# Kernel tuning notes

Measured on AMD Instinct MI355X. Metric: run time of the kernel, lower is better.

Reference implementation:

```python
import jax, jax.numpy as jnp
import numpy as np

# Problem dims (see shape_source)
T, H, FFN, K, E = 2048, 1024, 2048, 4, 32
LOCAL_EXPERT_IDS = (0, 8, 16, 24)  # round_robin plan: E=32, ep_size=8, ep_rank=0
N_LOCAL = len(LOCAL_EXPERT_IDS)
W_INIT = 0.02


def setup_inputs() -> dict:
    key = jax.random.key(0)
    k1, k2, k3, k4, k5 = jax.random.split(key, 5)
    hidden_2d = jax.random.normal(k1, (T, H), jnp.float32)
    selected_experts = jax.random.randint(k2, (T, K), 0, E)          # int routing ids
    routing_weights = jax.random.uniform(k3, (T, K), jnp.float32)    # nonneg gate probs
    gate_up_stack = jax.random.normal(k4, (N_LOCAL, 2 * FFN, H), jnp.float32) * W_INIT
    down_stack = jax.random.normal(k5, (N_LOCAL, H, FFN), jnp.float32) * W_INIT
    return {
        "hidden_2d": hidden_2d,
        "selected_experts": selected_experts,
        "routing_weights": routing_weights,
        "gate_up_stack": gate_up_stack,
        "down_stack": down_stack,
    }


def reference(hidden_2d, selected_experts, routing_weights, gate_up_stack, down_stack):
    """JAX port of ShardedExperts.forward_local.

    Same math as the torch sort/gather grouped-GEMM path: for every
    (token, k) assignment whose expert id is local, compute
    down(silu(gate) * up) and scatter-add routing_weight * out into the
    token row. Expressed densely per local expert (fixed small loop),
    which is the jit-friendly equivalent: the per-token expert weight
    w_e[t] = sum_k routing_weights[t,k] * [selected[t,k] == e] collapses
    duplicate assignments exactly like index_add_ does.
    """
    partial = jnp.zeros_like(hidden_2d)
    for i, eid in enumerate(LOCAL_EXPERT_IDS):
        # [T] combined routing weight for this expert (0 for unrouted tokens)
        w_e = jnp.sum(routing_weights * (selected_experts == eid), axis=-1)
        gu = hidden_2d @ gate_up_stack[i].T          # [T, 2*FFN]
        gate, up = jnp.split(gu, 2, axis=-1)         # gu.chunk(2, dim=-1)
        h = jax.nn.silu(gate) * up                   # act_fn(gate) * up
        out = h @ down_stack[i].T                    # [T, H]
        partial = partial + out * w_e[:, None]
    return partial
```

## Files before the change

kernel.cpp:

```cpp
#include <hip/hip_runtime.h>
#include <cstdint>
#include <cstddef>

#define TT  2048
#define HH  1024
#define FFN 2048
#define NL  4
#define BK  64
#define BM  256
#define SK  2

typedef __attribute__((ext_vector_type(8))) short bf16x8;
typedef __attribute__((ext_vector_type(4))) unsigned short u16x4;
typedef __attribute__((ext_vector_type(4))) float f32x4;

__device__ __forceinline__ unsigned short f2bf(float f) {
  unsigned u = __builtin_bit_cast(unsigned, f);
  u += 0x7FFFu + ((u >> 16) & 1u);
  return (unsigned short)(u >> 16);
}

__device__ __forceinline__ bf16x8 pack8(f32x4 f0, f32x4 f1) {
  bf16x8 v;
  v[0] = (short)f2bf(f0[0]); v[1] = (short)f2bf(f0[1]);
  v[2] = (short)f2bf(f0[2]); v[3] = (short)f2bf(f0[3]);
  v[4] = (short)f2bf(f1[0]); v[5] = (short)f2bf(f1[1]);
  v[6] = (short)f2bf(f1[2]); v[7] = (short)f2bf(f1[3]);
  return v;
}

__device__ __forceinline__ u16x4 pack4(f32x4 f0) {
  u16x4 v;
  v[0] = f2bf(f0[0]); v[1] = f2bf(f0[1]);
  v[2] = f2bf(f0[2]); v[3] = f2bf(f0[3]);
  return v;
}

__device__ __forceinline__ void async16(void* lds, const void* g) {
  __builtin_amdgcn_global_load_lds(
      (const __attribute__((address_space(1))) unsigned int*)g,
      (__attribute__((address_space(3))) unsigned int*)lds, 16, 0, 0);
}

__device__ __forceinline__ int swz(int b) { return b ^ (((b >> 7) & 7) << 4); }

__device__ __forceinline__ void lds_barrier() {
  asm volatile("s_waitcnt lgkmcnt(0)" ::: "memory");
  __builtin_amdgcn_s_barrier();
}

__global__ void k_zero(float* __restrict__ out, int* __restrict__ cnt) {
  int i = blockIdx.x * 256 + threadIdx.x;
  f32x4 z = {0.f, 0.f, 0.f, 0.f};
  reinterpret_cast<f32x4*>(out)[i] = z;
  if (i < NL) cnt[i] = 0;
}

__global__ void k_build(const int* __restrict__ sel, const float* __restrict__ rw,
                        int* __restrict__ cnt, int* __restrict__ tok,
                        float* __restrict__ wgt) {
  int t = blockIdx.x * 256 + threadIdx.x;
  if (t >= TT) return;
  int   s0 = sel[t*4+0], s1 = sel[t*4+1], s2 = sel[t*4+2], s3 = sel[t*4+3];
  float r0 = rw[t*4+0],  r1 = rw[t*4+1],  r2 = rw[t*4+2],  r3 = rw[t*4+3];
#pragma unroll
  for (int i = 0; i < NL; ++i) {
    int eid = i * 8;
    float w = 0.f; bool m = false;
    if (s0 == eid) { w += r0; m = true; }
    if (s1 == eid) { w += r1; m = true; }
    if (s2 == eid) { w += r2; m = true; }
    if (s3 == eid) { w += r3; m = true; }
    if (m) {
      int p = atomicAdd(&cnt[i], 1);
      tok[i*TT + p] = t;
      wgt[i*TT + p] = w;
    }
  }
}

__global__ void k_gather(const float* __restrict__ hidden, const int* __restrict__ cnt,
                         const int* __restrict__ tok, unsigned short* __restrict__ X) {
  int p = blockIdx.x, e = blockIdx.y;
  if (p >= cnt[e]) return;
  int t = tok[e*TT + p];
  const f32x4* src = reinterpret_cast<const f32x4*>(hidden + (size_t)t * HH);
  f32x4 a = src[threadIdx.x*2], b = src[threadIdx.x*2 + 1];
  reinterpret_cast<bf16x8*>(X + ((size_t)e*TT + p) * HH)[threadIdx.x] = pack8(a, b);
}

__global__ __launch_bounds__(512) void k_gemm1(
    const unsigned short* __restrict__ X, const float* __restrict__ gup,
    const int* __restrict__ cnt, unsigned short* __restrict__ Hb) {
  int bid = blockIdx.x;
  int xcd = bid & 7;
  int e   = xcd >> 1;
  int idx = (bid >> 3) * 2 + (xcd & 1);
  int n0  = idx * 32;
  int c   = cnt[e];

  __shared__ alignas(16) unsigned short As[3][BM*BK];
  __shared__ alignas(16) unsigned short Bs[2][64*BK];

  int tid  = threadIdx.x;
  int lane = tid & 63, wv = tid >> 6;
  int lr = lane & 15,  lk = lane >> 4;
  int wm = wv >> 1,    wn = wv & 1;

  const unsigned short* Ab = X   + (size_t)e * TT * HH;
  const float*          Gb = gup + (size_t)e * 2 * FFN * HH;

  int arow[4], acol[4], dstA[4];
#pragma unroll
  for (int cc = 0; cc < 4; ++cc) {
    int chunk = wv * 4 + cc;
    int P = chunk * 1024 + lane * 16;
    arow[cc] = P >> 7;
    acol[cc] = (P & 127) ^ ((arow[cc] & 7) << 4);
    dstA[cc] = P;
  }

  int rb  = tid >> 3;
  int cbf = (tid & 7) * 8;
  int grow = (rb < 32) ? (n0 + rb) : (FFN + n0 + rb - 32);
  const float* gB = Gb + (size_t)grow * HH + cbf;
  int wb = swz(rb * 128 + cbf * 2);

  int aoff[4][2], bgo[2], buo[2];
#pragma unroll
  for (int mi = 0; mi < 4; ++mi)
#pragma unroll
    for (int kk = 0; kk < 2; ++kk)
      aoff[mi][kk] = swz((wm*64 + mi*16 + lr) * 128 + kk*64 + lk*16);
#pragma unroll
  for (int kk = 0; kk < 2; ++kk) {
    bgo[kk] = swz((wn*16 + lr) * 128 + kk*64 + lk*16);
    buo[kk] = swz((32 + wn*16 + lr) * 128 + kk*64 + lk*16);
  }

  const int NT = HH / BK;

  for (int m0 = 0; m0 < c; m0 += BM) {
    __syncthreads();

    const char* srcA[4];
#pragma unroll
    for (int cc = 0; cc < 4; ++cc)
      srcA[cc] = (const char*)(Ab + (size_t)(m0 + arow[cc]) * HH) + acol[cc];

    f32x4 accg[4], accu[4];
    f32x4 z = {0.f, 0.f, 0.f, 0.f};
#pragma unroll
    for (int a = 0; a < 4; ++a) { accg[a] = z; accu[a] = z; }

    f32x4 br[2][2];

#pragma unroll
    for (int cc = 0; cc < 4; ++cc) async16((char*)As[0] + dstA[cc], srcA[cc]);
    br[0][0] = *(const f32x4*)(gB);
    br[0][1] = *(const f32x4*)(gB + 4);
    *(bf16x8*)((char*)Bs[0] + wb) = pack8(br[0][0], br[0][1]);
#pragma unroll
    for (int cc = 0; cc < 4; ++cc) async16((char*)As[1] + dstA[cc], srcA[cc] + BK*2);
    br[1][0] = *(const f32x4*)(gB + BK);
    br[1][1] = *(const f32x4*)(gB + BK + 4);
    lds_barrier();

#pragma unroll
    for (int t = 0; t < NT; ++t) {
      if (t + 2 < NT) {
        int k2 = (t + 2) * BK;
#pragma unroll
        for (int cc = 0; cc < 4; ++cc)
          async16((char*)As[(t+2)%3] + dstA[cc], srcA[cc] + k2*2);
        br[t & 1][0] = *(const f32x4*)(gB + k2);
        br[t & 1][1] = *(const f32x4*)(gB + k2 + 4);
      }
      __builtin_amdgcn_sched_barrier(0);
      if (t + 1 < NT)
        *(bf16x8*)((char*)Bs[(t+1) & 1] + wb) = pack8(br[(t+1) & 1][0], br[(t+1) & 1][1]);
      {
        const char* Asc = (const char*)As[t % 3];
        const char* Bsc = (const char*)Bs[t & 1];
#pragma unroll
        for (int kk = 0; kk < 2; ++kk) {
          bf16x8 bg = *(const bf16x8*)(Bsc + bgo[kk]);
          bf16x8 bu = *(const bf16x8*)(Bsc + buo[kk]);
#pragma unroll
          for (int mi = 0; mi < 4; ++mi) {
            bf16x8 a = *(const bf16x8*)(Asc + aoff[mi][kk]);
            accg[mi] = __builtin_amdgcn_mfma_f32_16x16x32_bf16(a, bg, accg[mi], 0, 0, 0);
            accu[mi] = __builtin_amdgcn_mfma_f32_16x16x32_bf16(a, bu, accu[mi], 0, 0, 0);
          }
        }
      }
      if (t + 1 < NT) lds_barrier();
    }

#pragma unroll
    for (int mi = 0; mi < 4; ++mi)
#pragma unroll
      for (int j = 0; j < 4; ++j) {
        int p = m0 + wm*64 + mi*16 + lk*4 + j;
        if (p < c) {
          float gv = accg[mi][j];
          float hv = (gv / (1.f + __expf(-gv))) * accu[mi][j];
          Hb[((size_t)e * TT + p) * FFN + (n0 + wn*16 + lr)] = f2bf(hv);
        }
      }
  }
}

__global__ __launch_bounds__(512) void k_gemm2(
    const unsigned short* __restrict__ Hb, const float* __restrict__ down,
    const int* __restrict__ cnt, float* __restrict__ part) {
  int bid = blockIdx.x;
  int xcd = bid & 7;
  int e   = xcd >> 1;
  int idx = (bid >> 3) * 2 + (xcd & 1);
  int sk  = idx >> 5;
  int n0  = (idx & 31) * 32;
  int c   = cnt[e];
  int kbase = sk * (FFN / SK);

  __shared__ alignas(16) unsigned short As[3][BM*BK];
  __shared__ alignas(16) unsigned short Bs[2][32*BK];

  int tid  = threadIdx.x;
  int lane = tid & 63, wv = tid >> 6;
  int lr = lane & 15,  lk = lane >> 4;
  int wm = wv >> 1,    wn = wv & 1;

  const unsigned short* Ab = Hb   + (size_t)e * TT * FFN;
  const float*          Db = down + (size_t)e * HH * FFN;

  int arow[4], acol[4], dstA[4];
#pragma unroll
  for (int cc = 0; cc < 4; ++cc) {
    int chunk = wv * 4 + cc;
    int P = chunk * 1024 + lane * 16;
    arow[cc] = P >> 7;
    acol[cc] = (P & 127) ^ ((arow[cc] & 7) << 4);
    dstA[cc] = P;
  }

  int rb  = tid >> 4;
  int cbf = (tid & 15) * 4;
  const float* gB = Db + (size_t)(n0 + rb) * FFN + kbase + cbf;
  int wb = swz(rb * 128 + cbf * 2);

  int aoff[4][2], boff[2];
#pragma unroll
  for (int mi = 0; mi < 4; ++mi)
#pragma unroll
    for (int kk = 0; kk < 2; ++kk)
      aoff[mi][kk] = swz((wm*64 + mi*16 + lr) * 128 + kk*64 + lk*16);
#pragma unroll
  for (int kk = 0; kk < 2; ++kk)
    boff[kk] = swz((wn*16 + lr) * 128 + kk*64 + lk*16);

  float* pBase = part + (size_t)(sk * NL + e) * TT * HH;
  const int NT = (FFN / SK) / BK;

  for (int m0 = 0; m0 < c; m0 += BM) {
    __syncthreads();

    const char* srcA[4];
#pragma unroll
    for (int cc = 0; cc < 4; ++cc)
      srcA[cc] = (const char*)(Ab + (size_t)(m0 + arow[cc]) * FFN + kbase) + acol[cc];

    f32x4 acc[4];
    f32x4 z = {0.f, 0.f, 0.f, 0.f};
#pragma unroll
    for (int a = 0; a < 4; ++a) acc[a] = z;

    f32x4 br[2];

#pragma unroll
    for (int cc = 0; cc < 4; ++cc) async16((char*)As[0] + dstA[cc], srcA[cc]);
    br[0] = *(const f32x4*)(gB);
    *(u16x4*)((char*)Bs[0] + wb) = pack4(br[0]);
#pragma unroll
    for (int cc = 0; cc < 4; ++cc) async16((char*)As[1] + dstA[cc], srcA[cc] + BK*2);
    br[1] = *(const f32x4*)(gB + BK);
    lds_barrier();

#pragma unroll
    for (int t = 0; t < NT; ++t) {
      if (t + 2 < NT) {
        int k2 = (t + 2) * BK;
#pragma unroll
        for (int cc = 0; cc < 4; ++cc)
          async16((char*)As[(t+2)%3] + dstA[cc], srcA[cc] + k2*2);
        br[t & 1] = *(const f32x4*)(gB + k2);
      }
      __builtin_amdgcn_sched_barrier(0);
      if (t + 1 < NT)
        *(u16x4*)((char*)Bs[(t+1) & 1] + wb) = pack4(br[(t+1) & 1]);
      {
        const char* Asc = (const char*)As[t % 3];
        const char* Bsc = (const char*)Bs[t & 1];
#pragma unroll
        for (int kk = 0; kk < 2; ++kk) {
          bf16x8 bf_ = *(const bf16x8*)(Bsc + boff[kk]);
#pragma unroll
          for (int mi = 0; mi < 4; ++mi) {
            bf16x8 a = *(const bf16x8*)(Asc + aoff[mi][kk]);
            acc[mi] = __builtin_amdgcn_mfma_f32_16x16x32_bf16(a, bf_, acc[mi], 0, 0, 0);
          }
        }
      }
      if (t + 1 < NT) lds_barrier();
    }

#pragma unroll
    for (int mi = 0; mi < 4; ++mi)
#pragma unroll
      for (int j = 0; j < 4; ++j) {
        int p = m0 + wm*64 + mi*16 + lk*4 + j;
        pBase[(size_t)p * HH + (n0 + wn*16 + lr)] = acc[mi][j];
      }
  }
}

__global__ __launch_bounds__(256) void k_combine(
    const float* __restrict__ part, const int* __restrict__ cnt,
    const int* __restrict__ tok, const float* __restrict__ wgt,
    float* __restrict__ out) {
  int bid = blockIdx.x;
  int e   = bid >> 8;
  int ps  = bid & 255;
  int c   = cnt[e];
  int col = threadIdx.x * 4;
  const size_t skStride = (size_t)NL * TT * HH;

  for (int p = ps; p < c; p += 256) {
    int   t = tok[e*TT + p];
    float w = wgt[e*TT + p];
    const float* base = part + ((size_t)e * TT + p) * HH + col;
    f32x4 s = *(const f32x4*)(base);
    s += *(const f32x4*)(base + skStride);
    float* o = out + (size_t)t * HH + col;
    atomicAdd(o+0, w*s[0]); atomicAdd(o+1, w*s[1]);
    atomicAdd(o+2, w*s[2]); atomicAdd(o+3, w*s[3]);
  }
}

extern "C" void kernel_launch(void* const* d_in, const int* in_sizes, int n_in,
                              void* d_out, int out_size, void* d_ws, size_t ws_size,
                              hipStream_t stream) {
  const float* hidden = (const float*)d_in[0];
  const int*   sel    = (const int*)d_in[1];
  const float* rw     = (const float*)d_in[2];
  const float* gup    = (const float*)d_in[3];
  const float* dwn    = (const float*)d_in[4];
  float* out = (float*)d_out;

  char* ws = (char*)d_ws;
  int*            cnt  = (int*)ws;
  int*            tok  = (int*)(ws + 1024);
  float*          wgt  = (float*)(ws + 33792);
  unsigned short* X    = (unsigned short*)(ws + 66560);
  unsigned short* Hb   = (unsigned short*)(ws + 16843776);
  float*          part = (float*)(ws + 50398208);

  k_zero   <<<2048, 256, 0, stream>>>(out, cnt);
  k_build  <<<8,    256, 0, stream>>>(sel, rw, cnt, tok, wgt);
  k_gather <<<dim3(TT, NL), 128, 0, stream>>>(hidden, cnt, tok, X);
  k_gemm1  <<<256, 512, 0, stream>>>(X, gup, cnt, Hb);
  k_gemm2  <<<256, 512, 0, stream>>>(Hb, dwn, cnt, part);
  k_combine<<<1024, 256, 0, stream>>>(part, cnt, tok, wgt, out);
}
```

Baseline: 68.11 us.

## Fuse combine into down-projection GEMM epilogue and drop split-K

Removes the split-K partial buffer and the separate combine kernel. gemm2 now covers the full FFN reduction per block with 16-column N tiles and scatters weighted results straight into the output through atomics in its epilogue. This avoids writing and re-reading the large fp32 partial tensor and saves one launch. In exchange each block does a longer K loop with fewer MFMAs per wave, and the atomics are scalar and strided, which may be less coalesced than the old vectorised combine.

```diff
diff --git a/kernel.cpp b/kernel.cpp
--- a/kernel.cpp
+++ b/kernel.cpp
@@ -8,11 +8,11 @@
 #define NL  4
 #define BK  64
 #define BM  256
-#define SK  2
 
 typedef __attribute__((ext_vector_type(8))) short bf16x8;
 typedef __attribute__((ext_vector_type(4))) unsigned short u16x4;
 typedef __attribute__((ext_vector_type(4))) float f32x4;
+typedef __attribute__((ext_vector_type(2))) float f32x2;
 
 __device__ __forceinline__ unsigned short f2bf(float f) {
   unsigned u = __builtin_bit_cast(unsigned, f);
@@ -29,11 +29,8 @@
   return v;
 }
 
-__device__ __forceinline__ u16x4 pack4(f32x4 f0) {
-  u16x4 v;
-  v[0] = f2bf(f0[0]); v[1] = f2bf(f0[1]);
-  v[2] = f2bf(f0[2]); v[3] = f2bf(f0[3]);
-  return v;
+__device__ __forceinline__ unsigned pack2(f32x2 f) {
+  return (unsigned)f2bf(f[0]) | ((unsigned)f2bf(f[1]) << 16);
 }
 
 __device__ __forceinline__ void async16(void* lds, const void* g) {
@@ -213,23 +210,21 @@
 
 __global__ __launch_bounds__(512) void k_gemm2(
     const unsigned short* __restrict__ Hb, const float* __restrict__ down,
-    const int* __restrict__ cnt, float* __restrict__ part) {
+    const int* __restrict__ cnt, const int* __restrict__ tok,
+    const float* __restrict__ wgt, float* __restrict__ out) {
   int bid = blockIdx.x;
   int xcd = bid & 7;
   int e   = xcd >> 1;
   int idx = (bid >> 3) * 2 + (xcd & 1);
-  int sk  = idx >> 5;
-  int n0  = (idx & 31) * 32;
+  int n0  = idx * 16;
   int c   = cnt[e];
-  int kbase = sk * (FFN / SK);
 
   __shared__ alignas(16) unsigned short As[3][BM*BK];
-  __shared__ alignas(16) unsigned short Bs[2][32*BK];
+  __shared__ alignas(16) unsigned short Bs[2][16*BK];
 
   int tid  = threadIdx.x;
   int lane = tid & 63, wv = tid >> 6;
   int lr = lane & 15,  lk = lane >> 4;
-  int wm = wv >> 1,    wn = wv & 1;
 
   const unsigned short* Ab = Hb   + (size_t)e * TT * FFN;
   const float*          Db = down + (size_t)e * HH * FFN;
@@ -244,23 +239,22 @@
     dstA[cc] = P;
   }
 
-  int rb  = tid >> 4;
-  int cbf = (tid & 15) * 4;
-  const float* gB = Db + (size_t)(n0 + rb) * FFN + kbase + cbf;
-  int wb = swz(rb * 128 + cbf * 2);
-
-  int aoff[4][2], boff[2];
-#pragma unroll
-  for (int mi = 0; mi < 4; ++mi)
+  int rb = tid >> 5;
+  int cw = tid & 31;
+  const float* gB = Db + (size_t)(n0 + rb) * FFN + cw*2;
+  int wb = swz(rb * 128 + cw * 4);
+
+  int aoff[2][2], boff[2];
+#pragma unroll
+  for (int mi = 0; mi < 2; ++mi)
 #pragma unroll
     for (int kk = 0; kk < 2; ++kk)
-      aoff[mi][kk] = swz((wm*64 + mi*16 + lr) * 128 + kk*64 + lk*16);
+      aoff[mi][kk] = swz((wv*32 + mi*16 + lr) * 128 + kk*64 + lk*16);
 #pragma unroll
   for (int kk = 0; kk < 2; ++kk)
-    boff[kk] = swz((wn*16 + lr) * 128 + kk*64 + lk*16);
-
-  float* pBase = part + (size_t)(sk * NL + e) * TT * HH;
-  const int NT = (FFN / SK) / BK;
+    boff[kk] = swz((lr) * 128 + kk*64 + lk*16);
+
+  const int NT = FFN / BK;
 
   for (int m0 = 0; m0 < c; m0 += BM) {
     __syncthreads();
@@ -268,22 +262,21 @@
     const char* srcA[4];
 #pragma unroll
     for (int cc = 0; cc < 4; ++cc)
-      srcA[cc] = (const char*)(Ab + (size_t)(m0 + arow[cc]) * FFN + kbase) + acol[cc];
-
-    f32x4 acc[4];
+      srcA[cc] = (const char*)(Ab + (size_t)(m0 + arow[cc]) * FFN) + acol[cc];
+
+    f32x4 acc[2];
     f32x4 z = {0.f, 0.f, 0.f, 0.f};
-#pragma unroll
-    for (int a = 0; a < 4; ++a) acc[a] = z;
-
-    f32x4 br[2];
+    acc[0] = z; acc[1] = z;
+
+    f32x2 br[2];
 
 #pragma unroll
     for (int cc = 0; cc < 4; ++cc) async16((char*)As[0] + dstA[cc], srcA[cc]);
-    br[0] = *(const f32x4*)(gB);
-    *(u16x4*)((char*)Bs[0] + wb) = pack4(br[0]);
+    br[0] = *(const f32x2*)(gB);
+    *(unsigned*)((char*)Bs[0] + wb) = pack2(br[0]);
 #pragma unroll
     for (int cc = 0; cc < 4; ++cc) async16((char*)As[1] + dstA[cc], srcA[cc] + BK*2);
-    br[1] = *(const f32x4*)(gB + BK);
+    br[1] = *(const f32x2*)(gB + BK);
     lds_barrier();
 
 #pragma unroll
@@ -293,11 +286,11 @@
 #pragma unroll
         for (int cc = 0; cc < 4; ++cc)
           async16((char*)As[(t+2)%3] + dstA[cc], srcA[cc] + k2*2);
-        br[t & 1] = *(const f32x4*)(gB + k2);
+        br[t & 1] = *(const f32x2*)(gB + k2);
       }
       __builtin_amdgcn_sched_barrier(0);
       if (t + 1 < NT)
-        *(u16x4*)((char*)Bs[(t+1) & 1] + wb) = pack4(br[(t+1) & 1]);
+        *(unsigned*)((char*)Bs[(t+1) & 1] + wb) = pack2(br[(t+1) & 1]);
       {
         const char* Asc = (const char*)As[t % 3];
         const char* Bsc = (const char*)Bs[t & 1];
@@ -305,7 +298,7 @@
         for (int kk = 0; kk < 2; ++kk) {
           bf16x8 bf_ = *(const bf16x8*)(Bsc + boff[kk]);
 #pragma unroll
-          for (int mi = 0; mi < 4; ++mi) {
+          for (int mi = 0; mi < 2; ++mi) {
             bf16x8 a = *(const bf16x8*)(Asc + aoff[mi][kk]);
             acc[mi] = __builtin_amdgcn_mfma_f32_16x16x32_bf16(a, bf_, acc[mi], 0, 0, 0);
           }
@@ -315,35 +308,16 @@
     }
 
 #pragma unroll
-    for (int mi = 0; mi < 4; ++mi)
+    for (int mi = 0; mi < 2; ++mi)
 #pragma unroll
       for (int j = 0; j < 4; ++j) {
-        int p = m0 + wm*64 + mi*16 + lk*4 + j;
-        pBase[(size_t)p * HH + (n0 + wn*16 + lr)] = acc[mi][j];
-      }
-  }
-}
-
-__global__ __launch_bounds__(256) void k_combine(
-    const float* __restrict__ part, const int* __restrict__ cnt,
-    const int* __restrict__ tok, const float* __restrict__ wgt,
-    float* __restrict__ out) {
-  int bid = blockIdx.x;
-  int e   = bid >> 8;
-  int ps  = bid & 255;
-  int c   = cnt[e];
-  int col = threadIdx.x * 4;
-  const size_t skStride = (size_t)NL * TT * HH;
-
-  for (int p = ps; p < c; p += 256) {
-    int   t = tok[e*TT + p];
-    float w = wgt[e*TT + p];
-    const float* base = part + ((size_t)e * TT + p) * HH + col;
-    f32x4 s = *(const f32x4*)(base);
-    s += *(const f32x4*)(base + skStride);
-    float* o = out + (size_t)t * HH + col;
-    atomicAdd(o+0, w*s[0]); atomicAdd(o+1, w*s[1]);
-    atomicAdd(o+2, w*s[2]); atomicAdd(o+3, w*s[3]);
+        int p = m0 + wv*32 + mi*16 + lk*4 + j;
+        if (p < c) {
+          int   t = tok[e*TT + p];
+          float w = wgt[e*TT + p];
+          atomicAdd(&out[(size_t)t * HH + (n0 + lr)], w * acc[mi][j]);
+        }
+      }
   }
 }
 
@@ -363,12 +337,10 @@
   float*          wgt  = (float*)(ws + 33792);
   unsigned short* X    = (unsigned short*)(ws + 66560);
   unsigned short* Hb   = (unsigned short*)(ws + 16843776);
-  float*          part = (float*)(ws + 50398208);
-
-  k_zero   <<<2048, 256, 0, stream>>>(out, cnt);
-  k_build  <<<8,    256, 0, stream>>>(sel, rw, cnt, tok, wgt);
-  k_gather <<<dim3(TT, NL), 128, 0, stream>>>(hidden, cnt, tok, X);
-  k_gemm1  <<<256, 512, 0, stream>>>(X, gup, cnt, Hb);
-  k_gemm2  <<<256, 512, 0, stream>>>(Hb, dwn, cnt, part);
-  k_combine<<<1024, 256, 0, stream>>>(part, cnt, tok, wgt, out);
-}
+
+  k_zero  <<<2048, 256, 0, stream>>>(out, cnt);
+  k_build <<<8,    256, 0, stream>>>(sel, rw, cnt, tok, wgt);
+  k_gather<<<dim3(TT, NL), 128, 0, stream>>>(hidden, cnt, tok, X);
+  k_gemm1 <<<256, 512, 0, stream>>>(X, gup, cnt, Hb);
+  k_gemm2 <<<256, 512, 0, stream>>>(Hb, dwn, cnt, tok, wgt, out);
+}
```

Result: faster. 61.69 us (-9.4%).
